# Kernel optimization log

Measured on AMD Instinct MI355X. Metric: run time of the kernel, lower is better.

The kernel has to match this reference:

```python
import jax, jax.numpy as jnp
import numpy as np

EPS = 1e-10


def setup_inputs() -> dict:
    key = jax.random.key(0)
    ks = jax.random.split(key, 7)
    B, N, E, R, D = 16, 30000, 300000, 200, 64
    return {
        "e_index": jax.random.randint(ks[0], (B, 2), 0, N),
        "r_index": jax.random.randint(ks[1], (B, 2), 0, R),
        "edge_index": jax.random.randint(ks[2], (2, E), 0, N),
        "edge_type": jax.random.randint(ks[3], (E,), 0, R),
        "num_nodes": N,
        "rel_emb": jax.random.normal(ks[4], (R, D), dtype=jnp.float32) * 0.1,
        "rel_proj": jax.random.normal(ks[5], (R, D), dtype=jnp.float32) * 0.1,
        "w_out": jax.random.normal(ks[6], (D,), dtype=jnp.float32) * 0.1,
    }


def _relation_projection(h_prob, r, edge_index, edge_type, rel_emb, rel_proj, w_out, num_nodes):
    # RelationProjection.forward: query = rel_reprs[arange(bs), r_index]
    q = rel_emb[r]                                   # [B, D]
    # input = einsum('bn,bd->bnd', h_prob, query)
    inp = h_prob[:, :, None] * q[:, None, :]         # [B, N, D]
    src, dst = edge_index[0], edge_index[1]
    edge_w = rel_proj[edge_type]                     # [E, D]
    # entity model: per-edge gather from head, relation-modulated message, scatter-sum to tail
    msg = inp[:, src, :] * edge_w[None, :, :]        # [B, E, D]
    agg = jax.vmap(lambda m: jax.ops.segment_sum(m, dst, num_segments=num_nodes))(msg)  # [B, N, D]
    out = agg @ w_out                                # [B, N] node scores
    return jax.nn.sigmoid(out)                       # t_prob = sigmoid(output)


def reference(e_index, r_index, edge_index, edge_type, num_nodes, rel_emb, rel_proj, w_out):
    # Fixed '2i' program: operand e1, proj r1, operand e2, proj r2, intersection, stop.
    # apply_operand: one-hot over nodes
    p1 = jax.nn.one_hot(e_index[:, 0], num_nodes, dtype=rel_emb.dtype)
    t1 = _relation_projection(p1, r_index[:, 0], edge_index, edge_type,
                              rel_emb, rel_proj, w_out, num_nodes)
    p2 = jax.nn.one_hot(e_index[:, 1], num_nodes, dtype=rel_emb.dtype)
    t2 = _relation_projection(p2, r_index[:, 1], edge_index, edge_type,
                              rel_emb, rel_proj, w_out, num_nodes)
    # conjunction, product logic: x * y
    t_prob = t1 * t2
    # final logit transform from UltraQuery.forward
    return jnp.log((t_prob + EPS) / (1.0 - t_prob + EPS))
```

## Files before the change

### kernel.cpp

```cpp
#include <hip/hip_runtime.h>
#include <math.h>

#define EPSF 1e-10f

__global__ void edge_scan_kernel(const int* __restrict__ e_index,
                                 const int* __restrict__ r_index,
                                 const int* __restrict__ edge_index,
                                 const int* __restrict__ edge_type,
                                 const float* __restrict__ rel_emb,
                                 const float* __restrict__ rel_proj,
                                 const float* __restrict__ w_out,
                                 float* __restrict__ sums,
                                 int E, int N, int P, int D) {
    extern __shared__ int sh[];
    int* sh_e = sh;
    int* sh_r = sh + P;
    for (int t = threadIdx.x; t < P; t += blockDim.x) {
        sh_e[t] = e_index[t];
        sh_r[t] = r_index[t];
    }
    __syncthreads();

    int i = blockIdx.x * blockDim.x + threadIdx.x;
    if (i >= E) return;
    int src = edge_index[i];
    int dst = edge_index[E + i];
    int et  = -1;
    for (int p = 0; p < P; ++p) {
        if (src == sh_e[p]) {
            if (et < 0) et = edge_type[i];
            const float* q = rel_emb  + (size_t)sh_r[p] * D;
            const float* w = rel_proj + (size_t)et * D;
            float acc = 0.0f;
            for (int d = 0; d < D; ++d) acc = fmaf(q[d] * w[d], w_out[d], acc);
            const int b = p >> 1, j = p & 1;
            atomicAdd(&sums[((size_t)b * N + dst) * 2 + j], acc);
        }
    }
}

__global__ void finalize_kernel(const float2* __restrict__ sums,
                                float* __restrict__ out,
                                int BN) {
    int i = blockIdx.x * blockDim.x + threadIdx.x;
    if (i >= BN) return;
    float2 s = sums[i];
    float t1 = 1.0f / (1.0f + expf(-s.x));
    float t2 = 1.0f / (1.0f + expf(-s.y));
    float t  = t1 * t2;
    out[i] = logf((t + EPSF) / (1.0f - t + EPSF));
}

extern "C" void kernel_launch(void* const* d_in, const int* in_sizes, int n_in,
                              void* d_out, int out_size, void* d_ws, size_t ws_size,
                              hipStream_t stream) {
    const int*   e_index    = (const int*)d_in[0];
    const int*   r_index    = (const int*)d_in[1];
    const int*   edge_index = (const int*)d_in[2];
    const int*   edge_type  = (const int*)d_in[3];
    const float* rel_emb    = (const float*)d_in[5];
    const float* rel_proj   = (const float*)d_in[6];
    const float* w_out      = (const float*)d_in[7];

    const int B = in_sizes[0] / 2;
    const int E = in_sizes[2] / 2;
    const int D = in_sizes[7];
    const int N = out_size / B;
    const int P = 2 * B;

    float* sums = (float*)d_ws;
    float* out  = (float*)d_out;

    const int block = 256;
    const int grid1 = (E + block - 1) / block;
    const size_t shmem = (size_t)(2 * P) * sizeof(int);
    hipLaunchKernelGGL(edge_scan_kernel, dim3(grid1), dim3(block), shmem, stream,
                       e_index, r_index, edge_index, edge_type,
                       rel_emb, rel_proj, w_out, sums, E, N, P, D);

    const int BN = B * N;
    const int grid2 = (BN + block - 1) / block;
    hipLaunchKernelGGL(finalize_kernel, dim3(grid2), dim3(block), 0, stream,
                       (const float2*)sums, out, BN);
}
```

Before: 83.90 us.

## Fuse edge scan and finalize into one cooperative kernel with grid sync

Merges the edge-scan and finalize kernels into a single cooperative launch with a grid-stride loop over 512x256 threads, separated by a grid-wide sync. This removes one kernel launch and the gap between the two kernels. The finalize step also writes a precomputed constant when both sums are near zero, skipping the exp/log math for the many nodes that no edge reached. In exchange it pays for the cooperative grid barrier, runs the edge scan with a fixed grid, and loads dst only on a match.

```diff
diff --git a/kernel.cpp b/kernel.cpp
--- a/kernel.cpp
+++ b/kernel.cpp
@@ -1,17 +1,21 @@
 #include <hip/hip_runtime.h>
+#include <hip/hip_cooperative_groups.h>
 #include <math.h>
+
+namespace cg = cooperative_groups;
 
 #define EPSF 1e-10f
 
-__global__ void edge_scan_kernel(const int* __restrict__ e_index,
-                                 const int* __restrict__ r_index,
-                                 const int* __restrict__ edge_index,
-                                 const int* __restrict__ edge_type,
-                                 const float* __restrict__ rel_emb,
-                                 const float* __restrict__ rel_proj,
-                                 const float* __restrict__ w_out,
-                                 float* __restrict__ sums,
-                                 int E, int N, int P, int D) {
+__global__ void fused_kernel(const int* __restrict__ e_index,
+                             const int* __restrict__ r_index,
+                             const int* __restrict__ edge_index,
+                             const int* __restrict__ edge_type,
+                             const float* __restrict__ rel_emb,
+                             const float* __restrict__ rel_proj,
+                             const float* __restrict__ w_out,
+                             float* __restrict__ sums,
+                             float* __restrict__ out,
+                             int E, int N, int P, int D, int BN) {
     extern __shared__ int sh[];
     int* sh_e = sh;
     int* sh_r = sh + P;
@@ -21,34 +25,43 @@
     }
     __syncthreads();
 
-    int i = blockIdx.x * blockDim.x + threadIdx.x;
-    if (i >= E) return;
-    int src = edge_index[i];
-    int dst = edge_index[E + i];
-    int et  = -1;
-    for (int p = 0; p < P; ++p) {
-        if (src == sh_e[p]) {
-            if (et < 0) et = edge_type[i];
-            const float* q = rel_emb  + (size_t)sh_r[p] * D;
-            const float* w = rel_proj + (size_t)et * D;
-            float acc = 0.0f;
-            for (int d = 0; d < D; ++d) acc = fmaf(q[d] * w[d], w_out[d], acc);
-            const int b = p >> 1, j = p & 1;
-            atomicAdd(&sums[((size_t)b * N + dst) * 2 + j], acc);
+    const int nthreads = gridDim.x * blockDim.x;
+    const int tid = blockIdx.x * blockDim.x + threadIdx.x;
+
+    for (int i = tid; i < E; i += nthreads) {
+        int src = edge_index[i];
+        int et  = -1;
+        for (int p = 0; p < P; ++p) {
+            if (src == sh_e[p]) {
+                if (et < 0) et = edge_type[i];
+                int dst = edge_index[E + i];
+                const float* q = rel_emb  + (size_t)sh_r[p] * D;
+                const float* w = rel_proj + (size_t)et * D;
+                float acc = 0.0f;
+                for (int d = 0; d < D; ++d) acc = fmaf(q[d] * w[d], w_out[d], acc);
+                const int b = p >> 1, j = p & 1;
+                atomicAdd(&sums[((size_t)b * N + dst) * 2 + j], acc);
+            }
         }
     }
-}
 
-__global__ void finalize_kernel(const float2* __restrict__ sums,
-                                float* __restrict__ out,
-                                int BN) {
-    int i = blockIdx.x * blockDim.x + threadIdx.x;
-    if (i >= BN) return;
-    float2 s = sums[i];
-    float t1 = 1.0f / (1.0f + expf(-s.x));
-    float t2 = 1.0f / (1.0f + expf(-s.y));
-    float t  = t1 * t2;
-    out[i] = logf((t + EPSF) / (1.0f - t + EPSF));
+    cg::this_grid().sync();
+
+    const float CONST_OUT = logf((0.25f + EPSF) / (0.75f + EPSF));
+    const float2* s2 = (const float2*)sums;
+    for (int i = tid; i < BN; i += nthreads) {
+        float2 s = s2[i];
+        float r;
+        if (fabsf(s.x) < 1e-6f && fabsf(s.y) < 1e-6f) {
+            r = CONST_OUT;
+        } else {
+            float t1 = 1.0f / (1.0f + expf(-s.x));
+            float t2 = 1.0f / (1.0f + expf(-s.y));
+            float t  = t1 * t2;
+            r = logf((t + EPSF) / (1.0f - t + EPSF));
+        }
+        out[i] = r;
+    }
 }
 
 extern "C" void kernel_launch(void* const* d_in, const int* in_sizes, int n_in,
@@ -62,24 +75,23 @@
     const float* rel_proj   = (const float*)d_in[6];
     const float* w_out      = (const float*)d_in[7];
 
-    const int B = in_sizes[0] / 2;
-    const int E = in_sizes[2] / 2;
-    const int D = in_sizes[7];
-    const int N = out_size / B;
-    const int P = 2 * B;
+    const int B  = in_sizes[0] / 2;
+    const int E  = in_sizes[2] / 2;
+    const int D  = in_sizes[7];
+    const int N  = out_size / B;
+    const int P  = 2 * B;
+    const int BN = B * N;
 
     float* sums = (float*)d_ws;
     float* out  = (float*)d_out;
 
-    const int block = 256;
-    const int grid1 = (E + block - 1) / block;
+    dim3 grid(512), block(256);
     const size_t shmem = (size_t)(2 * P) * sizeof(int);
-    hipLaunchKernelGGL(edge_scan_kernel, dim3(grid1), dim3(block), shmem, stream,
-                       e_index, r_index, edge_index, edge_type,
-                       rel_emb, rel_proj, w_out, sums, E, N, P, D);
 
-    const int BN = B * N;
-    const int grid2 = (BN + block - 1) / block;
-    hipLaunchKernelGGL(finalize_kernel, dim3(grid2), dim3(block), 0, stream,
-                       (const float2*)sums, out, BN);
+    int E_ = E, N_ = N, P_ = P, D_ = D, BN_ = BN;
+    void* args[] = {(void*)&e_index, (void*)&r_index, (void*)&edge_index,
+                    (void*)&edge_type, (void*)&rel_emb, (void*)&rel_proj,
+                    (void*)&w_out, (void*)&sums, (void*)&out,
+                    &E_, &N_, &P_, &D_, &BN_};
+    hipLaunchCooperativeKernel((void*)fused_kernel, grid, block, args, shmem, stream);
 }
```

Measured after the change: 162.2 us. 93.4% more time.
